# Kernel optimization log

Hardware: AMD Instinct MI355X
Metric: run time of the kernel (lower is better)

## Reference

```python
import jax, jax.numpy as jnp
import numpy as np

THRESH = 0.1        # spike_threshold
GRAD_WIDTH = 1.0    # width_grad
GRAD_SCALE = 1.0    # scale_grad

# SingleSpike with SingleExponential surrogate gradient (sinabs/EXODUS semantics)
@jax.custom_vjp
def single_spike(v):
    return (v >= THRESH).astype(v.dtype)

def _spk_fwd(v):
    return single_spike(v), v

def _spk_bwd(v, g):
    abs_width = GRAD_WIDTH * THRESH
    surr = (GRAD_SCALE / abs_width) * jnp.exp(-jnp.abs(v - THRESH) / abs_width)
    return (g * surr,)

single_spike.defvjp(_spk_fwd, _spk_bwd)

def weight_norm(v, g):
    # torch weight_norm: w = g * v / ||v|| with norm over all dims except dim 0
    norm = jnp.sqrt(jnp.sum(v * v, axis=tuple(range(1, v.ndim)), keepdims=True))
    return g.reshape((-1,) + (1,) * (v.ndim - 1)) * v / norm

def conv2d_same(x, w):
    return jax.lax.conv_general_dilated(
        x, w, window_strides=(1, 1), padding='SAME',
        dimension_numbers=('NCHW', 'OIHW', 'NCHW'))

def avg_pool2(x):
    s = jax.lax.reduce_window(x, 0.0, jax.lax.add, (1, 1, 2, 2), (1, 1, 2, 2), 'VALID')
    return s * 0.25

def iaf_squeeze(syn, batch_size):
    # syn: (B*T, C, H, W); IAFSqueeze: unflatten time, integrate-and-fire recurrence,
    # single spike per step, membrane-subtract reset, re-flatten.
    bt = syn.shape[0]
    t = bt // batch_size
    syn = syn.reshape(batch_size, t, *syn.shape[1:])
    def step(v, inp):
        v = v + inp
        s = single_spike(v)
        return v - THRESH * s, s
    v0 = jnp.zeros_like(syn[:, 0])
    _, spikes = jax.lax.scan(step, v0, jnp.moveaxis(syn, 1, 0))  # (T, B, C, H, W)
    out = jnp.moveaxis(spikes, 0, 1)
    return out.reshape(bt, *out.shape[2:])

def _forward(x, conv_params, lin_v, lin_g):
    b, t = x.shape[0], x.shape[1]
    h = x.reshape(b * t, *x.shape[2:])  # flatten(0,1)
    for v, g in conv_params:
        h = iaf_squeeze(conv2d_same(h, weight_norm(v, g)), b)
        if h.shape[-1] > 4:
            h = avg_pool2(h)
    w = weight_norm(lin_v, lin_g)           # (11, C*4*4)
    out = h.reshape(b * t, -1) @ w.T        # (B*T, 11)
    return out.reshape(b, t, out.shape[-1])

def setup_inputs() -> dict:
    key = jax.random.key(0)
    ks = jax.random.split(key, 6)
    B, T, H = 32, 50, 64
    chans = [2, 8, 16, 32, 64]
    d = {'x': jax.random.uniform(ks[0], (B, T, 2, H, H), dtype=jnp.float32)}
    for i in range(4):
        d[f'conv{i}_v'] = jax.random.normal(ks[1 + i], (chans[i + 1], chans[i], 3, 3), jnp.float32)
        d[f'conv{i}_g'] = jnp.ones((chans[i + 1],), jnp.float32)
    d['lin_v'] = jax.random.normal(ks[5], (11, 64 * 4 * 4), jnp.float32)
    d['lin_g'] = jnp.ones((11,), jnp.float32)
    return d

def reference(x, conv0_v, conv0_g, conv1_v, conv1_g, conv2_v, conv2_g, conv3_v, conv3_g, lin_v, lin_g):
    conv_params = [(conv0_v, conv0_g), (conv1_v, conv1_g), (conv2_v, conv2_g), (conv3_v, conv3_g)]
    return _forward(x, conv_params, lin_v, lin_g)
```

## Files before the change

kernel.cpp:

```cpp
#include <hip/hip_runtime.h>

#define THRESH 0.1f

typedef float    f4 __attribute__((ext_vector_type(4)));
typedef float    f2 __attribute__((ext_vector_type(2)));
typedef _Float16 h8 __attribute__((ext_vector_type(8)));
typedef _Float16 h4 __attribute__((ext_vector_type(4)));
typedef _Float16 h2 __attribute__((ext_vector_type(2)));

__global__ void wnorm_all(const float* __restrict__ c0v, const float* __restrict__ c0g,
                          const float* __restrict__ c1v, const float* __restrict__ c1g,
                          const float* __restrict__ c2v, const float* __restrict__ c2g,
                          const float* __restrict__ c3v, const float* __restrict__ c3g,
                          const float* __restrict__ lv,  const float* __restrict__ lg,
                          float* __restrict__ w0, float* __restrict__ w1,
                          float* __restrict__ w2, float* __restrict__ w3,
                          float* __restrict__ wl) {
    int rb = blockIdx.x;
    const float *v, *g; float* w; int fanin, row;
    if (rb < 8)        { v = c0v; g = c0g; w = w0; fanin = 18;   row = rb; }
    else if (rb < 24)  { v = c1v; g = c1g; w = w1; fanin = 72;   row = rb - 8; }
    else if (rb < 56)  { v = c2v; g = c2g; w = w2; fanin = 144;  row = rb - 24; }
    else if (rb < 120) { v = c3v; g = c3g; w = w3; fanin = 288;  row = rb - 56; }
    else               { v = lv;  g = lg;  w = wl; fanin = 1024; row = rb - 120; }
    const bool perm = (rb >= 120);

    const float* vr = v + (size_t)row * fanin;
    float ss = 0.f;
    for (int i = threadIdx.x; i < fanin; i += 64) { float x = vr[i]; ss = fmaf(x, x, ss); }
    #pragma unroll
    for (int off = 32; off > 0; off >>= 1) ss += __shfl_down(ss, off);
    ss = __shfl(ss, 0);
    float scale = g[row] / sqrtf(ss);
    float* wr = w + (size_t)row * fanin;
    for (int i = threadIdx.x; i < fanin; i += 64) {
        int d = perm ? (((i & 15) << 6) | (i >> 4)) : i;
        wr[d] = vr[i] * scale;
    }
}

template<int CIN, int H, int COUT, int CG, int WX, int SEGS, int BDIM, int PSB>
__launch_bounds__(BDIM)
__global__ void conv_iaf_pool(const void* __restrict__ in_, const float* __restrict__ w,
                              _Float16* __restrict__ out, int B, int T) {
    constexpr bool HIN  = (CIN % 8 == 0);
    constexpr int Hp    = H / 2;
    constexpr int PP    = Hp * Hp;
    constexpr int HH    = H * H;
    constexpr int WY    = 64 / WX;
    constexpr int NW    = BDIM / 64;
    constexpr int NWps  = NW / SEGS;
    constexpr int XW    = H / WX;
    constexpr int YWV   = NWps / XW;
    constexpr int RPB   = YWV * WY;
    constexpr int STRIPS= H / RPB;
    constexpr int CGRP  = COUT / (CG * SEGS);
    constexpr int SR    = RPB + 2;
    constexpr int COLS  = H + 2;
    constexpr int SLABB = SR * COLS * PSB;
    constexpr bool FULLY= (RPB == H);
    constexpr int R0    = FULLY ? 1 : 0;
    constexpr int NR    = FULLY ? H : SR;
    constexpr int UPC   = HIN ? (CIN / 8) : 1;
    constexpr int NU    = NR * H * UPC;
    constexpr int ITERS = (NU + BDIM - 1) / BDIM;
    constexpr bool GUARD= !(FULLY && (NU % BDIM == 0));

    __shared__ alignas(16) char slab[2][SLABB];

    const int tid = threadIdx.x;
    const int G = gridDim.x, bx = blockIdx.x;
    const int pb = (bx & 7) * (G >> 3) + (bx >> 3);
    const int cgb   = pb % CGRP;
    const int strip = (pb / CGRP) % STRIPS;
    const int b     = pb / (CGRP * STRIPS);

    const int wid = tid >> 6, l = tid & 63;
    const int seg = wid / NWps;
    const int wlv = wid % NWps;
    const int xw = wlv % XW, yw = wlv / XW;
    const int xl = l % WX, ylw = l / WX;
    const int x  = xw * WX + xl;
    const int yy = yw * WY + ylw;
    const int y0 = strip * RPB;
    const int y  = y0 + yy;

    const int c0 = __builtin_amdgcn_readfirstlane((cgb * SEGS + seg) * CG);
    const float* __restrict__ wu = w + (size_t)c0 * (CIN * 9);

    int addrB[9];
    #pragma unroll
    for (int dr = 0; dr < 3; ++dr)
        #pragma unroll
        for (int dc = 0; dc < 3; ++dc)
            addrB[dr * 3 + dc] = ((yy + dr) * COLS + (x + dc)) * PSB;

    int goff[ITERS], loffB[ITERS];
    #pragma unroll
    for (int i = 0; i < ITERS; ++i) {
        const int idx = tid + i * BDIM;
        int j, gx, rr0;
        if constexpr (HIN) { j = idx % UPC; gx = (idx / UPC) % H; rr0 = idx / (UPC * H); }
        else               { j = 0;         gx = idx % H;         rr0 = (idx / H) % NR; }
        const int rr = R0 + rr0;
        const int gy = y0 - 1 + rr;
        const bool ok = (idx < NU) && ((unsigned)gy < (unsigned)H);
        if constexpr (HIN) goff[i] = ok ? ((gy * H + gx) * UPC + j) : -1;
        else               goff[i] = ok ? (gy * H + gx) : -1;
        loffB[i] = ok ? ((rr * COLS + (gx + 1)) * PSB + 16 * j) : -1;
    }

    constexpr bool WREG = !HIN && (CG * CIN * 9) <= 80;
    float wreg[WREG ? (CG * CIN * 9) : 1];
    if constexpr (WREG) {
        #pragma unroll
        for (int i = 0; i < CG * CIN * 9; ++i) wreg[i] = wu[i];
    }

    for (int i = tid; i < (2 * SLABB) / 4; i += BDIM) ((int*)slab)[i] = 0;
    __syncthreads();

    float vmem[CG];
    #pragma unroll
    for (int c = 0; c < CG; ++c) vmem[c] = 0.f;

    f4 pf[ITERS];
    #define GATHER(t_)                                                            \
        if constexpr (HIN) {                                                      \
            const f4* inb = (const f4*)in_ + (size_t)(b * T + (t_)) * (HH * UPC); \
            _Pragma("unroll")                                                     \
            for (int i = 0; i < ITERS; ++i) {                                     \
                f4 r_ = {0.f, 0.f, 0.f, 0.f};                                     \
                if (!GUARD || goff[i] >= 0) r_ = inb[goff[i]];                    \
                pf[i] = r_;                                                       \
            }                                                                     \
        } else {                                                                  \
            const float* inb = (const float*)in_ + (size_t)(b * T + (t_)) * (CIN * HH); \
            _Pragma("unroll")                                                     \
            for (int i = 0; i < ITERS; ++i) {                                     \
                f4 r_ = {0.f, 0.f, 0.f, 0.f};                                     \
                if (goff[i] >= 0) { r_.x = inb[goff[i]]; r_.y = inb[goff[i] + HH]; } \
                pf[i] = r_;                                                       \
            }                                                                     \
        }
    #define STAGE(buf)                                                            \
        _Pragma("unroll")                                                         \
        for (int i = 0; i < ITERS; ++i) {                                         \
            if (!GUARD || loffB[i] >= 0) {                                        \
                if constexpr (HIN) *(f4*)(&slab[buf][loffB[i]]) = pf[i];          \
                else { f2 v2_; v2_.x = pf[i].x; v2_.y = pf[i].y;                  \
                       *(f2*)(&slab[buf][loffB[i]]) = v2_; }                      \
            }                                                                     \
        }

    {
        GATHER(0)
        STAGE(0)
        GATHER(1)
    }
    __syncthreads();

    for (int t = 0; t < T; ++t) {
        if (t + 1 < T) { STAGE((t + 1) & 1) }
        if (t + 2 < T) { GATHER(t + 2) }

        const char* sb = slab[t & 1];
        float acc[CG];
        #pragma unroll
        for (int c = 0; c < CG; ++c) acc[c] = 0.f;

        if constexpr (HIN) {
            #pragma unroll
            for (int o = 0; o < CIN / 8; ++o) {
                h8 P[9];
                #pragma unroll
                for (int k = 0; k < 9; ++k)
                    P[k] = *(const h8*)(sb + addrB[k] + 16 * o);
                #pragma unroll
                for (int cid = 0; cid < 8; ++cid) {
                    const int ci = 8 * o + cid;
                    #pragma unroll
                    for (int c = 0; c < CG; ++c)
                        #pragma unroll
                        for (int k = 0; k < 9; ++k)
                            acc[c] = fmaf((float)P[k][cid],
                                          wu[(size_t)(c * CIN + ci) * 9 + k], acc[c]);
                }
            }
        } else {
            f2 P[9];
            #pragma unroll
            for (int k = 0; k < 9; ++k)
                P[k] = *(const f2*)(sb + addrB[k]);
            #pragma unroll
            for (int cid = 0; cid < 2; ++cid)
                #pragma unroll
                for (int c = 0; c < CG; ++c)
                    #pragma unroll
                    for (int k = 0; k < 9; ++k)
                        acc[c] = fmaf(P[k][cid],
                                      WREG ? wreg[(c * CIN + cid) * 9 + k]
                                           : wu[(size_t)(c * CIN + cid) * 9 + k],
                                      acc[c]);
        }

        float sv[CG];
        #pragma unroll
        for (int c = 0; c < CG; ++c) {
            vmem[c] += acc[c];
            float s = (vmem[c] >= THRESH) ? 1.f : 0.f;
            vmem[c] -= THRESH * s;
            float sum = s;
            sum += __shfl_xor(sum, 1);
            sum += __shfl_xor(sum, WX);
            sv[c] = 0.25f * sum;
        }
        if (((xl | ylw) & 1) == 0) {
            const size_t ob = ((size_t)(b * T + t) * PP + (y >> 1) * Hp + (x >> 1)) * COUT + c0;
            if constexpr (CG == 4) {
                h4 hv = {(_Float16)sv[0], (_Float16)sv[1], (_Float16)sv[2], (_Float16)sv[3]};
                *(h4*)(out + ob) = hv;
            } else if constexpr (CG == 2) {
                h2 hv = {(_Float16)sv[0], (_Float16)sv[1]};
                *(h2*)(out + ob) = hv;
            } else {
                out[ob] = (_Float16)sv[0];
            }
        }
        __syncthreads();
    }
    #undef GATHER
    #undef STAGE
}

__global__ void linear_kernel(const _Float16* __restrict__ h, const float* __restrict__ w,
                              float* __restrict__ out) {
    __shared__ float hs[1024];
    __shared__ float part[16][17];
    const int n = blockIdx.x;
    for (int i = threadIdx.x; i < 1024; i += blockDim.x)
        hs[i] = (float)h[(size_t)n * 1024 + i];
    __syncthreads();
    const int j = threadIdx.x & 15, ch = threadIdx.x >> 4;
    float acc = 0.f;
    if (j < 11) {
        const float* wr = w + (size_t)j * 1024 + ch * 64;
        const float* hh = hs + ch * 64;
        #pragma unroll 8
        for (int k = 0; k < 64; ++k) acc = fmaf(hh[k], wr[k], acc);
    }
    part[j][ch] = acc;
    __syncthreads();
    if (threadIdx.x < 11) {
        float s = 0.f;
        #pragma unroll
        for (int cc = 0; cc < 16; ++cc) s += part[threadIdx.x][cc];
        out[(size_t)n * 11 + threadIdx.x] = s;
    }
}

extern "C" void kernel_launch(void* const* d_in, const int* in_sizes, int n_in,
                              void* d_out, int out_size, void* d_ws, size_t ws_size,
                              hipStream_t stream) {
    const int B = 32, T = 50;

    const float* x   = (const float*)d_in[0];
    const float* c0v = (const float*)d_in[1];
    const float* c0g = (const float*)d_in[2];
    const float* c1v = (const float*)d_in[3];
    const float* c1g = (const float*)d_in[4];
    const float* c2v = (const float*)d_in[5];
    const float* c2g = (const float*)d_in[6];
    const float* c3v = (const float*)d_in[7];
    const float* c3g = (const float*)d_in[8];
    const float* lv  = (const float*)d_in[9];
    const float* lg  = (const float*)d_in[10];
    float* out = (float*)d_out;

    float* ws = (float*)d_ws;
    float* w0 = ws;
    float* w1 = w0 + 144;
    float* w2 = w1 + 1152;
    float* w3 = w2 + 4608;
    float* wl = w3 + 18432;
    _Float16* bufA16 = (_Float16*)(ws + 40960);
    _Float16* bufB16 = (_Float16*)(ws + 40960 + 13107200);

    wnorm_all<<<131, 64, 0, stream>>>(c0v, c0g, c1v, c1g, c2v, c2g, c3v, c3g,
                                      lv, lg, w0, w1, w2, w3, wl);

    conv_iaf_pool<2,  64, 8,  4, 32, 1, 256, 8 ><<<1024, 256, 0, stream>>>(x,       w0, bufA16, B, T);
    conv_iaf_pool<8,  32, 16, 4, 32, 1, 256, 16><<<512,  256, 0, stream>>>(bufA16,  w1, bufB16, B, T);
    conv_iaf_pool<16, 16, 32, 2, 16, 2, 256, 48><<<512,  256, 0, stream>>>(bufB16,  w2, bufA16, B, T);
    conv_iaf_pool<32, 8,  64, 1, 8,  4, 256, 80><<<512,  256, 0, stream>>>(bufA16,  w3, bufB16, B, T);

    linear_kernel<<<B * T, 256, 0, stream>>>(bufB16, wl, out);
}
```

Before: 551.2 us.

## Use single-wavefront blocks per conv tile to drop block barriers

```diff
diff --git a/kernel.cpp b/kernel.cpp
--- a/kernel.cpp
+++ b/kernel.cpp
@@ -39,8 +39,8 @@
     }
 }
 
-template<int CIN, int H, int COUT, int CG, int WX, int SEGS, int BDIM, int PSB>
-__launch_bounds__(BDIM)
+template<int CIN, int H, int COUT, int CG, int WX, int PSB>
+__launch_bounds__(64, 4)
 __global__ void conv_iaf_pool(const void* __restrict__ in_, const float* __restrict__ w,
                               _Float16* __restrict__ out, int B, int T) {
     constexpr bool HIN  = (CIN % 8 == 0);
@@ -48,44 +48,39 @@
     constexpr int PP    = Hp * Hp;
     constexpr int HH    = H * H;
     constexpr int WY    = 64 / WX;
-    constexpr int NW    = BDIM / 64;
-    constexpr int NWps  = NW / SEGS;
     constexpr int XW    = H / WX;
-    constexpr int YWV   = NWps / XW;
-    constexpr int RPB   = YWV * WY;
-    constexpr int STRIPS= H / RPB;
-    constexpr int CGRP  = COUT / (CG * SEGS);
-    constexpr int SR    = RPB + 2;
-    constexpr int COLS  = H + 2;
+    constexpr int STRIPS= H / WY;
+    constexpr int CGRP  = COUT / CG;
+    constexpr int SR    = WY + 2;
+    constexpr int COLS  = (XW == 1) ? (H + 2) : (WX + 2);
     constexpr int SLABB = SR * COLS * PSB;
-    constexpr bool FULLY= (RPB == H);
+    constexpr bool FULLY= (WY == H);
     constexpr int R0    = FULLY ? 1 : 0;
-    constexpr int NR    = FULLY ? H : SR;
+    constexpr int NRR   = FULLY ? H : SR;
+    constexpr int SCN   = (XW == 1) ? H : (WX + 2);
     constexpr int UPC   = HIN ? (CIN / 8) : 1;
-    constexpr int NU    = NR * H * UPC;
-    constexpr int ITERS = (NU + BDIM - 1) / BDIM;
-    constexpr bool GUARD= !(FULLY && (NU % BDIM == 0));
+    constexpr int NU    = NRR * SCN * UPC;
+    constexpr int UN    = (NU + 63) / 64;
+    constexpr bool GUARD= !(FULLY && (NU % 64 == 0));
 
     __shared__ alignas(16) char slab[2][SLABB];
 
-    const int tid = threadIdx.x;
+    const int l = threadIdx.x;
     const int G = gridDim.x, bx = blockIdx.x;
-    const int pb = (bx & 7) * (G >> 3) + (bx >> 3);
-    const int cgb   = pb % CGRP;
-    const int strip = (pb / CGRP) % STRIPS;
-    const int b     = pb / (CGRP * STRIPS);
-
-    const int wid = tid >> 6, l = tid & 63;
-    const int seg = wid / NWps;
-    const int wlv = wid % NWps;
-    const int xw = wlv % XW, yw = wlv / XW;
+    const int p = (bx & 7) * (G >> 3) + (bx >> 3);
+
+    const int cgb   = p % CGRP;
+    const int r1    = p / CGRP;
+    const int strip = r1 % STRIPS;
+    const int r2    = r1 / STRIPS;
+    const int xw    = r2 % XW;
+    const int b     = r2 / XW;
+
     const int xl = l % WX, ylw = l / WX;
-    const int x  = xw * WX + xl;
-    const int yy = yw * WY + ylw;
-    const int y0 = strip * RPB;
-    const int y  = y0 + yy;
-
-    const int c0 = __builtin_amdgcn_readfirstlane((cgb * SEGS + seg) * CG);
+    const int x0 = xw * WX, y0 = strip * WY;
+    const int x  = x0 + xl, y = y0 + ylw;
+
+    const int c0 = cgb * CG;
     const float* __restrict__ wu = w + (size_t)c0 * (CIN * 9);
 
     int addrB[9];
@@ -93,21 +88,24 @@
     for (int dr = 0; dr < 3; ++dr)
         #pragma unroll
         for (int dc = 0; dc < 3; ++dc)
-            addrB[dr * 3 + dc] = ((yy + dr) * COLS + (x + dc)) * PSB;
-
-    int goff[ITERS], loffB[ITERS];
-    #pragma unroll
-    for (int i = 0; i < ITERS; ++i) {
-        const int idx = tid + i * BDIM;
-        int j, gx, rr0;
-        if constexpr (HIN) { j = idx % UPC; gx = (idx / UPC) % H; rr0 = idx / (UPC * H); }
-        else               { j = 0;         gx = idx % H;         rr0 = (idx / H) % NR; }
-        const int rr = R0 + rr0;
+            addrB[dr * 3 + dc] = ((ylw + dr) * COLS + (xl + dc)) * PSB;
+
+    int goff[UN], loffB[UN];
+    #pragma unroll
+    for (int i = 0; i < UN; ++i) {
+        const int idx = l + i * 64;
+        int j, jx, ridx;
+        if constexpr (HIN) { j = idx % UPC; jx = (idx / UPC) % SCN; ridx = idx / (UPC * SCN); }
+        else               { j = 0;         jx = idx % SCN;         ridx = idx / SCN; }
+        const int rr = R0 + ridx;
         const int gy = y0 - 1 + rr;
-        const bool ok = (idx < NU) && ((unsigned)gy < (unsigned)H);
+        const int gx = (XW == 1) ? jx : (x0 - 1 + jx);
+        const int sc = (XW == 1) ? (jx + 1) : jx;
+        const bool ok = (idx < NU) && ((unsigned)gy < (unsigned)H) &&
+                        ((unsigned)gx < (unsigned)H);
         if constexpr (HIN) goff[i] = ok ? ((gy * H + gx) * UPC + j) : -1;
         else               goff[i] = ok ? (gy * H + gx) : -1;
-        loffB[i] = ok ? ((rr * COLS + (gx + 1)) * PSB + 16 * j) : -1;
+        loffB[i] = ok ? ((rr * COLS + sc) * PSB + 16 * j) : -1;
     }
 
     constexpr bool WREG = !HIN && (CG * CIN * 9) <= 80;
@@ -117,19 +115,18 @@
         for (int i = 0; i < CG * CIN * 9; ++i) wreg[i] = wu[i];
     }
 
-    for (int i = tid; i < (2 * SLABB) / 4; i += BDIM) ((int*)slab)[i] = 0;
-    __syncthreads();
+    for (int i = l; i < (2 * SLABB) / 4; i += 64) ((int*)slab)[i] = 0;
 
     float vmem[CG];
     #pragma unroll
     for (int c = 0; c < CG; ++c) vmem[c] = 0.f;
 
-    f4 pf[ITERS];
+    f4 pf[UN];
     #define GATHER(t_)                                                            \
         if constexpr (HIN) {                                                      \
             const f4* inb = (const f4*)in_ + (size_t)(b * T + (t_)) * (HH * UPC); \
             _Pragma("unroll")                                                     \
-            for (int i = 0; i < ITERS; ++i) {                                     \
+            for (int i = 0; i < UN; ++i) {                                        \
                 f4 r_ = {0.f, 0.f, 0.f, 0.f};                                     \
                 if (!GUARD || goff[i] >= 0) r_ = inb[goff[i]];                    \
                 pf[i] = r_;                                                       \
@@ -137,7 +134,7 @@
         } else {                                                                  \
             const float* inb = (const float*)in_ + (size_t)(b * T + (t_)) * (CIN * HH); \
             _Pragma("unroll")                                                     \
-            for (int i = 0; i < ITERS; ++i) {                                     \
+            for (int i = 0; i < UN; ++i) {                                        \
                 f4 r_ = {0.f, 0.f, 0.f, 0.f};                                     \
                 if (goff[i] >= 0) { r_.x = inb[goff[i]]; r_.y = inb[goff[i] + HH]; } \
                 pf[i] = r_;                                                       \
@@ -145,7 +142,7 @@
         }
     #define STAGE(buf)                                                            \
         _Pragma("unroll")                                                         \
-        for (int i = 0; i < ITERS; ++i) {                                         \
+        for (int i = 0; i < UN; ++i) {                                            \
             if (!GUARD || loffB[i] >= 0) {                                        \
                 if constexpr (HIN) *(f4*)(&slab[buf][loffB[i]]) = pf[i];          \
                 else { f2 v2_; v2_.x = pf[i].x; v2_.y = pf[i].y;                  \
@@ -158,7 +155,6 @@
         STAGE(0)
         GATHER(1)
     }
-    __syncthreads();
 
     for (int t = 0; t < T; ++t) {
         if (t + 1 < T) { STAGE((t + 1) & 1) }
@@ -227,7 +223,6 @@
                 out[ob] = (_Float16)sv[0];
             }
         }
-        __syncthreads();
     }
     #undef GATHER
     #undef STAGE
@@ -289,10 +284,10 @@
     wnorm_all<<<131, 64, 0, stream>>>(c0v, c0g, c1v, c1g, c2v, c2g, c3v, c3g,
                                       lv, lg, w0, w1, w2, w3, wl);
 
-    conv_iaf_pool<2,  64, 8,  4, 32, 1, 256, 8 ><<<1024, 256, 0, stream>>>(x,       w0, bufA16, B, T);
-    conv_iaf_pool<8,  32, 16, 4, 32, 1, 256, 16><<<512,  256, 0, stream>>>(bufA16,  w1, bufB16, B, T);
-    conv_iaf_pool<16, 16, 32, 2, 16, 2, 256, 48><<<512,  256, 0, stream>>>(bufB16,  w2, bufA16, B, T);
-    conv_iaf_pool<32, 8,  64, 1, 8,  4, 256, 80><<<512,  256, 0, stream>>>(bufA16,  w3, bufB16, B, T);
+    conv_iaf_pool<2,  64, 8,  4, 32, 8 ><<<4096, 64, 0, stream>>>(x,       w0, bufA16, B, T);
+    conv_iaf_pool<8,  32, 16, 4, 32, 16><<<2048, 64, 0, stream>>>(bufA16,  w1, bufB16, B, T);
+    conv_iaf_pool<16, 16, 32, 2, 16, 48><<<2048, 64, 0, stream>>>(bufB16,  w2, bufA16, B, T);
+    conv_iaf_pool<32, 8,  64, 1, 8,  80><<<2048, 64, 0, stream>>>(bufA16,  w3, bufB16, B, T);
 
     linear_kernel<<<B * T, 256, 0, stream>>>(bufB16, wl, out);
 }
```

New measurement: 585.2 us. +6.2%, slower.
